# Optimization experiments

Measured on AMD Instinct MI355X. Metric: run time of the kernel, lower is better.

Reference implementation:

```python
import jax, jax.numpy as jnp
import numpy as np

N, E, B, IN, DIM, H = 20000, 320000, 128, 25, 64, 8

def _lin(key, fin, fout):
    k1, k2 = jax.random.split(key)
    s = 1.0 / np.sqrt(fin)
    return (jax.random.uniform(k1, (fin, fout), jnp.float32, -s, s),
            jax.random.uniform(k2, (fout,), jnp.float32, -s, s))

def setup_inputs() -> dict:
    key = jax.random.key(0)
    ks = jax.random.split(key, 12)
    x = jax.random.normal(ks[0], (N, IN), jnp.float32)
    edge_index = jax.random.randint(ks[1], (2, E), 0, N, jnp.int64)
    batch = jnp.sort(jax.random.randint(ks[2], (N,), 0, B, jnp.int64))
    W0, b0 = _lin(ks[3], IN, DIM)
    Wg, _ = _lin(ks[4], DIM, H * DIM)            # GATConv lin (no bias)
    att_src = jax.random.normal(ks[5], (H, DIM), jnp.float32) * (1.0 / np.sqrt(DIM))
    att_dst = jax.random.normal(ks[6], (H, DIM), jnp.float32) * (1.0 / np.sqrt(DIM))
    bg = jnp.zeros((H * DIM,), jnp.float32)       # GATConv output bias
    Wh, bh = _lin(ks[7], H * DIM, DIM)            # head_nn
    sl = 1.0 / np.sqrt(DIM)
    W_ih = jax.random.uniform(ks[8], (4 * DIM, 2 * DIM), jnp.float32, -sl, sl)
    W_hh = jax.random.uniform(ks[9], (4 * DIM, DIM), jnp.float32, -sl, sl)
    b_ih = jnp.zeros((4 * DIM,), jnp.float32)
    b_hh = jnp.zeros((4 * DIM,), jnp.float32)
    W1, b1 = _lin(ks[10], 2 * DIM, DIM)
    W2, b2 = _lin(ks[11], DIM, 1)
    return dict(x=x, edge_index=edge_index, batch=batch, W0=W0, b0=b0, Wg=Wg,
                att_src=att_src, att_dst=att_dst, bg=bg, Wh=Wh, bh=bh,
                W_ih=W_ih, W_hh=W_hh, b_ih=b_ih, b_hh=b_hh, W1=W1, b1=b1, W2=W2, b2=b2)

def _forward(x, edge_index, batch, W0, b0, Wg, att_src, att_dst, bg, Wh, bh,
             W_ih, W_hh, b_ih, b_hh, W1, b1, W2, b2):
    n = x.shape[0]
    h0 = jax.nn.relu(x @ W0 + b0)                         # [N, DIM]
    xh = (h0 @ Wg).reshape(n, H, DIM)                     # [N, H, C]
    # add self-loops (PyG GATConv default)
    loop = jnp.arange(n, dtype=edge_index.dtype)
    src = jnp.concatenate([edge_index[0], loop])
    dst = jnp.concatenate([edge_index[1], loop])
    a_s = jnp.einsum('nhc,hc->nh', xh, att_src)           # [N, H]
    a_d = jnp.einsum('nhc,hc->nh', xh, att_dst)
    e = jax.nn.leaky_relu(a_s[src] + a_d[dst], 0.2)       # [Etot, H]
    m = jax.ops.segment_max(e, dst, num_segments=n)
    w = jnp.exp(e - m[dst])
    s = jax.ops.segment_sum(w, dst, num_segments=n)
    alpha = w / s[dst]                                    # segment softmax over dst
    agg = jax.ops.segment_sum(alpha[:, :, None] * xh[src], dst, num_segments=n)
    out = jax.nn.relu(agg.reshape(n, H * DIM) + bg)
    out = jax.nn.relu(out @ Wh + bh)                      # [N, DIM]
    # Set2Set, 3 processing steps
    q_star = jnp.zeros((B, 2 * DIM), out.dtype)
    h = jnp.zeros((B, DIM), out.dtype)
    c = jnp.zeros((B, DIM), out.dtype)
    for _ in range(3):
        g = q_star @ W_ih.T + b_ih + h @ W_hh.T + b_hh
        i_g, f_g, g_g, o_g = jnp.split(g, 4, axis=-1)
        c = jax.nn.sigmoid(f_g) * c + jax.nn.sigmoid(i_g) * jnp.tanh(g_g)
        h = jax.nn.sigmoid(o_g) * jnp.tanh(c)
        q = h                                             # [B, DIM]
        e2 = jnp.sum(out * q[batch], axis=-1)             # [N]
        m2 = jax.ops.segment_max(e2, batch, num_segments=B)
        w2 = jnp.exp(e2 - m2[batch])
        s2 = jax.ops.segment_sum(w2, batch, num_segments=B)
        a2 = w2 / s2[batch]
        r = jax.ops.segment_sum(a2[:, None] * out, batch, num_segments=B)
        q_star = jnp.concatenate([q, r], axis=-1)
    y = jax.nn.relu(q_star @ W1 + b1)
    y = y @ W2 + b2
    return y.reshape(-1)

def reference(x, edge_index, batch, W0, b0, Wg, att_src, att_dst, bg, Wh, bh,
              W_ih, W_hh, b_ih, b_hh, W1, b1, W2, b2):
    return _forward(x, edge_index, batch, W0, b0, Wg, att_src, att_dst, bg, Wh, bh,
                    W_ih, W_hh, b_ih, b_hh, W1, b1, W2, b2)
```

## Files before the change

### kernel.cpp

```cpp
#include <hip/hip_runtime.h>

#define N_NODES 20000
#define N_EDGES 320000
#define NBATCH  128

typedef __attribute__((ext_vector_type(8))) short s8v;
typedef __attribute__((ext_vector_type(4))) float f32x4;
typedef __attribute__((ext_vector_type(4))) int i32x4;

__device__ __forceinline__ float lrelu(float v) { return v > 0.f ? v : 0.2f * v; }
__device__ __forceinline__ float rdlane(float v, int l) {
    return __int_as_float(__builtin_amdgcn_readlane(__float_as_int(v), l));
}
__device__ __forceinline__ unsigned short bf16_rne(float f) {
    unsigned u = __float_as_uint(f);
    unsigned r = u + 0x7FFF + ((u >> 16) & 1);
    return (unsigned short)(r >> 16);
}

__global__ void k_small(const float* __restrict__ Wg, const float* __restrict__ Wh,
                        const float* __restrict__ att_s, const float* __restrict__ att_d,
                        float* __restrict__ vsd,
                        const int* __restrict__ batch, int* __restrict__ segst,
                        int* __restrict__ deg,
                        unsigned short* __restrict__ wgt_hi, unsigned short* __restrict__ wgt_lo,
                        unsigned short* __restrict__ wht_hi, unsigned short* __restrict__ wht_lo,
                        int n, int b) {
    int tid = threadIdx.x;
    int gid = blockIdx.x * 256 + tid;
    if (gid < n) deg[gid] = 0;
    if (blockIdx.x < 2) {
        int t = blockIdx.x * 256 + tid;
        int k = t >> 3, h = t & 7;
        const float* wrow = Wg + (size_t)k * 512 + h * 64;
        float s1 = 0.f, s2 = 0.f;
        #pragma unroll 8
        for (int c = 0; c < 64; c++) {
            float w = wrow[c];
            s1 += w * att_s[h * 64 + c];
            s2 += w * att_d[h * 64 + c];
        }
        vsd[k * 16 + h] = s1;
        vsd[k * 16 + 8 + h] = s2;
    } else if (blockIdx.x == 2) {
        if (tid > b) return;
        int lo = 0, hi = n;
        while (lo < hi) { int mid = (lo + hi) >> 1; if (batch[mid] < tid) lo = mid + 1; else hi = mid; }
        segst[tid] = lo;
    } else {
        int wi = (blockIdx.x - 3) * 256 + tid;
        int sel = wi >> 15;
        int r = wi & 32767;
        int h = r >> 12, nn = (r >> 6) & 63, k = r & 63;
        float val = (sel == 0) ? Wg[(size_t)k * 512 + h * 64 + nn]
                               : Wh[(size_t)(h * 64 + k) * 64 + nn];
        unsigned short hi = bf16_rne(val);
        float hf = __uint_as_float((unsigned)hi << 16);
        unsigned short lo = bf16_rne(val - hf);
        int o = h * 4096 + nn * 64 + k;
        if (sel == 0) { wgt_hi[o] = hi; wgt_lo[o] = lo; }
        else          { wht_hi[o] = hi; wht_lo[o] = lo; }
    }
}

__global__ void k_h0c(const float* __restrict__ x, const float* __restrict__ W0,
                      const float* __restrict__ b0, float* __restrict__ h0,
                      const int* __restrict__ edst, int* __restrict__ deg, int n) {
    __shared__ float ws[25 * 64];
    __shared__ float bs[64];
    __shared__ float xs[100];
    int t = threadIdx.x;
    if (t < 64) {
        int e = blockIdx.x * 64 + t;
        atomicAdd(&deg[edst[e]], 1);
    }
    for (int i = t; i < 25 * 64; i += 256) ws[i] = W0[i];
    if (t < 64) bs[t] = b0[t];
    int nb = blockIdx.x * 4;
    if (t < 100 && nb * 25 + t < n * 25) xs[t] = x[(size_t)nb * 25 + t];
    __syncthreads();
    int node = nb + (t >> 6);
    int c = t & 63;
    if (node >= n) return;
    float s = bs[c];
    const float* xr = xs + (t >> 6) * 25;
    #pragma unroll
    for (int k = 0; k < 25; k++) s += xr[k] * ws[k * 64 + c];
    h0[(size_t)node * 64 + c] = fmaxf(s, 0.f);
}

__global__ __launch_bounds__(256) void k_asd_scan(const float* __restrict__ h0,
                                                  const float* __restrict__ vsd,
                                                  float* __restrict__ a_s, float* __restrict__ a_d,
                                                  const int* __restrict__ deg,
                                                  int* __restrict__ tmp, int* __restrict__ bsum,
                                                  int nasd, int n) {
    __shared__ float hs[16][65];
    __shared__ float vl[64 * 16];
    __shared__ int wsum[4];
    int tid = threadIdx.x;
    if (blockIdx.x >= nasd) {
        int s = blockIdx.x - nasd;
        int i = s * 256 + tid;
        int lane = tid & 63, w = tid >> 6;
        int v = (i < n) ? deg[i] + 1 : 0;
        int x = v;
        #pragma unroll
        for (int off = 1; off < 64; off <<= 1) {
            int t2 = __shfl_up(x, off);
            if (lane >= off) x += t2;
        }
        if (lane == 63) wsum[w] = x;
        __syncthreads();
        int pre = 0;
        #pragma unroll
        for (int j = 0; j < 4; j++) if (j < w) pre += wsum[j];
        if (i < n) tmp[i] = pre + x - v;
        if (tid == 255) bsum[s] = pre + x;
        return;
    }
    int rbase = blockIdx.x * 16;
    {
        int row = tid / 16, c4 = (tid % 16) * 4;
        float4 hv = *(const float4*)(h0 + (size_t)(rbase + row) * 64 + c4);
        hs[row][c4] = hv.x; hs[row][c4 + 1] = hv.y; hs[row][c4 + 2] = hv.z; hs[row][c4 + 3] = hv.w;
    }
    #pragma unroll
    for (int j = 0; j < 4; j++) vl[tid + j * 256] = vsd[tid + j * 256];
    __syncthreads();
    int nl = tid / 16, o = tid % 16;
    float acc = 0.f;
    #pragma unroll 16
    for (int k = 0; k < 64; k++) acc += hs[nl][k] * vl[k * 16 + o];
    int node = rbase + nl;
    if (o < 8) a_s[node * 8 + o] = acc;
    else       a_d[node * 8 + (o - 8)] = acc;
}

__global__ void k_scan2(const int* __restrict__ tmp, const int* __restrict__ bsum,
                        int* __restrict__ offs, int* __restrict__ adj,
                        int* __restrict__ cursor, int n, int nblk) {
    int i = blockIdx.x * 256 + threadIdx.x;
    if (i > n) return;
    int b = i >> 8;
    int pre = 0;
    for (int j = 0; j < b; j++) pre += bsum[j];
    if (i == n) {
        int tot = pre;
        for (int j = b; j < nblk; j++) tot += bsum[j];
        offs[n] = tot;
        return;
    }
    int o = pre + tmp[i];
    offs[i] = o;
    adj[o] = i;
    cursor[i] = o + 1;
}

__global__ void k_fill_edge(const int* __restrict__ src, const int* __restrict__ dst,
                            int* __restrict__ cursor, int* __restrict__ adj, int e) {
    int i = blockIdx.x * 256 + threadIdx.x;
    if (i >= e) return;
    int p = atomicAdd(&cursor[dst[i]], 1);
    adj[p] = src[i];
}

__global__ __launch_bounds__(256) void k_gat6(const int* __restrict__ offs, const int* __restrict__ adj,
                                              const float* __restrict__ a_s, const float* __restrict__ a_d,
                                              const float* __restrict__ h0,
                                              float* __restrict__ agg_pre, int n) {
    int lane = threadIdx.x & 63;
    int node = blockIdx.x * 4 + (threadIdx.x >> 6);
    if (node >= n) return;
    int beg = offs[node], end = offs[node + 1];
    int g = lane >> 3, h = lane & 7;
    float ad = a_d[node * 8 + h];

    float m = -1e30f, s = 0.f;
    for (int i = beg + g; i < end; i += 8) {
        int src = adj[i];
        float e = lrelu(a_s[src * 8 + h] + ad);
        if (e > m) { s = s * __expf(m - e) + 1.f; m = e; }
        else       { s += __expf(e - m); }
    }
    #pragma unroll
    for (int off = 8; off < 64; off <<= 1) {
        float mo = __shfl_xor(m, off), so = __shfl_xor(s, off);
        float mn = fmaxf(m, mo);
        s = s * __expf(m - mn) + so * __expf(mo - mn);
        m = mn;
    }
    float rcp = 1.f / s;

    float acc[8] = {0.f, 0.f, 0.f, 0.f, 0.f, 0.f, 0.f, 0.f};
    for (int sbase = beg; sbase < end; sbase += 64) {
        int scnt = end - sbase; if (scnt > 64) scnt = 64;
        int srcv = 0;
        if (lane < scnt) srcv = adj[sbase + lane];
        float al[8];
        #pragma unroll
        for (int j = 0; j < 8; j++) {
            int q = j * 8 + g;
            float alv = 0.f;
            if (q < scnt) {
                int sq = __shfl(srcv, q);
                float e = lrelu(a_s[sq * 8 + h] + ad);
                alv = __expf(e - m) * rcp;
            }
            al[j] = alv;
        }
        #pragma unroll
        for (int j = 0; j < 8; j += 2) {
            int qb0 = j * 8, qb1 = (j + 1) * 8;
            if (qb0 >= scnt) break;
            bool has1 = qb1 < scnt;
            int sg0[8], sg1[8];
            float xv0[8], xv1[8];
            #pragma unroll
            for (int g2 = 0; g2 < 8; g2++) sg0[g2] = __builtin_amdgcn_readlane(srcv, qb0 + g2);
            #pragma unroll
            for (int g2 = 0; g2 < 8; g2++) sg1[g2] = __builtin_amdgcn_readlane(srcv, qb1 + g2);
            #pragma unroll
            for (int g2 = 0; g2 < 8; g2++) xv0[g2] = h0[(size_t)sg0[g2] * 64 + lane];
            if (has1) {
                #pragma unroll
                for (int g2 = 0; g2 < 8; g2++) xv1[g2] = h0[(size_t)sg1[g2] * 64 + lane];
            }
            #pragma unroll
            for (int g2 = 0; g2 < 8; g2++) {
                #pragma unroll
                for (int h2 = 0; h2 < 8; h2++)
                    acc[h2] += rdlane(al[j], g2 * 8 + h2) * xv0[g2];
            }
            if (has1) {
                #pragma unroll
                for (int g2 = 0; g2 < 8; g2++) {
                    #pragma unroll
                    for (int h2 = 0; h2 < 8; h2++)
                        acc[h2] += rdlane(al[j + 1], g2 * 8 + h2) * xv1[g2];
                }
            }
        }
    }
    #pragma unroll
    for (int h2 = 0; h2 < 8; h2++)
        agg_pre[(size_t)node * 512 + h2 * 64 + lane] = acc[h2];
}

__global__ __launch_bounds__(64) void k_fmma(const float* __restrict__ agg_pre,
                                             const unsigned short* __restrict__ wgt_hi,
                                             const unsigned short* __restrict__ wgt_lo,
                                             const unsigned short* __restrict__ wht_hi,
                                             const unsigned short* __restrict__ wht_lo,
                                             const float* __restrict__ bg,
                                             float* __restrict__ part, int M) {
    __shared__ unsigned C1[16 * 68];
    int lane = threadIdx.x;
    int m = lane & 15, quad = lane >> 4;
    int r0 = blockIdx.x * 16;
    int pair = blockIdx.y;
    f32x4 accO[4];
    #pragma unroll
    for (int i = 0; i < 4; i++) accO[i] = (f32x4){0.f, 0.f, 0.f, 0.f};

    #pragma unroll
    for (int hh = 0; hh < 2; hh++) {
        int h = pair * 2 + hh;
        s8v ahi[2], alo[2];
        #pragma unroll
        for (int ks = 0; ks < 2; ks++) {
            const float* ap = agg_pre + (size_t)(r0 + m) * 512 + h * 64 + ks * 32 + quad * 8;
            float av[8];
            *(float4*)&av[0] = *(const float4*)ap;
            *(float4*)&av[4] = *(const float4*)(ap + 4);
            #pragma unroll
            for (int j = 0; j < 8; j++) {
                unsigned short hi = bf16_rne(av[j]);
                float hf = __uint_as_float((unsigned)hi << 16);
                unsigned short lo = bf16_rne(av[j] - hf);
                ahi[ks][j] = (short)hi;
                alo[ks][j] = (short)lo;
            }
        }
        #pragma unroll
        for (int tn = 0; tn < 4; tn++) {
            f32x4 acc = (f32x4){0.f, 0.f, 0.f, 0.f};
            #pragma unroll
            for (int ks = 0; ks < 2; ks++) {
                const unsigned short* bp = wgt_hi + h * 4096 + (tn * 16 + m) * 64 + ks * 32 + quad * 8;
                const unsigned short* bl = wgt_lo + h * 4096 + (tn * 16 + m) * 64 + ks * 32 + quad * 8;
                s8v bhf = *(const s8v*)bp;
                s8v blf = *(const s8v*)bl;
                acc = __builtin_amdgcn_mfma_f32_16x16x32_bf16(alo[ks], bhf, acc, 0, 0, 0);
                acc = __builtin_amdgcn_mfma_f32_16x16x32_bf16(ahi[ks], blf, acc, 0, 0, 0);
                acc = __builtin_amdgcn_mfma_f32_16x16x32_bf16(ahi[ks], bhf, acc, 0, 0, 0);
            }
            float bgv = bg[h * 64 + tn * 16 + m];
            #pragma unroll
            for (int r = 0; r < 4; r++) {
                float v = fmaxf(acc[r] + bgv, 0.f);
                unsigned short hi = bf16_rne(v);
                float hf = __uint_as_float((unsigned)hi << 16);
                unsigned short lo = bf16_rne(v - hf);
                C1[(quad * 4 + r) * 68 + tn * 16 + m] = (unsigned)hi | ((unsigned)lo << 16);
            }
        }
        __syncthreads();
        s8v a2h[2], a2l[2];
        #pragma unroll
        for (int ks = 0; ks < 2; ks++) {
            const unsigned* cp = &C1[m * 68 + ks * 32 + quad * 8];
            unsigned uu[8];
            *(i32x4*)&uu[0] = *(const i32x4*)cp;
            *(i32x4*)&uu[4] = *(const i32x4*)(cp + 4);
            #pragma unroll
            for (int j = 0; j < 8; j++) {
                a2h[ks][j] = (short)(uu[j] & 0xFFFFu);
                a2l[ks][j] = (short)(uu[j] >> 16);
            }
        }
        #pragma unroll
        for (int tn = 0; tn < 4; tn++) {
            #pragma unroll
            for (int ks = 0; ks < 2; ks++) {
                const unsigned short* bp = wht_hi + h * 4096 + (tn * 16 + m) * 64 + ks * 32 + quad * 8;
                const unsigned short* bl = wht_lo + h * 4096 + (tn * 16 + m) * 64 + ks * 32 + quad * 8;
                s8v bhf = *(const s8v*)bp;
                s8v blf = *(const s8v*)bl;
                accO[tn] = __builtin_amdgcn_mfma_f32_16x16x32_bf16(a2l[ks], bhf, accO[tn], 0, 0, 0);
                accO[tn] = __builtin_amdgcn_mfma_f32_16x16x32_bf16(a2h[ks], blf, accO[tn], 0, 0, 0);
                accO[tn] = __builtin_amdgcn_mfma_f32_16x16x32_bf16(a2h[ks], bhf, accO[tn], 0, 0, 0);
            }
        }
        __syncthreads();
    }
    float* Cb = part + (size_t)pair * M * 64;
    #pragma unroll
    for (int tn = 0; tn < 4; tn++) {
        #pragma unroll
        for (int r = 0; r < 4; r++) {
            int row = r0 + quad * 4 + r;
            Cb[(size_t)row * 64 + tn * 16 + m] = accO[tn][r];
        }
    }
}

#define SROWS 208
__global__ __launch_bounds__(256) void k_s2s(const float* __restrict__ part,
                                             const float* __restrict__ bh,
                                             const int* __restrict__ segst,
                                             const float* __restrict__ W_ih, const float* __restrict__ W_hh,
                                             const float* __restrict__ b_ih, const float* __restrict__ b_hh,
                                             const float* __restrict__ W1, const float* __restrict__ b1,
                                             const float* __restrict__ W2, const float* __restrict__ b2,
                                             float* __restrict__ out, int M) {
    int b = blockIdx.x, tid = threadIdx.x, lane = tid & 63, w = tid >> 6;
    __shared__ float sc[SROWS * 65];
    __shared__ float wlds[1024];
    __shared__ float hl[64], cl[64], rl_[64];
    __shared__ float red[4];
    __shared__ float gsh[256];
    int beg = segst[b], end = segst[b + 1];
    int nrows = end - beg;
    int ncache = nrows < SROWS ? nrows : SROWS;
    const size_t PS = (size_t)M * 64;
    for (int idx = tid; idx < ncache * 16; idx += 256) {
        int r = idx >> 4, q = idx & 15;
        const float* pb = part + (size_t)(beg + r) * 64 + q * 4;
        float4 v0 = *(const float4*)pb;
        float4 v1 = *(const float4*)(pb + PS);
        float4 v2 = *(const float4*)(pb + 2 * PS);
        float4 v3 = *(const float4*)(pb + 3 * PS);
        float4 bv = *(const float4*)(bh + q * 4);
        float* p = &sc[r * 65 + q * 4];
        p[0] = fmaxf(v0.x + v1.x + v2.x + v3.x + bv.x, 0.f);
        p[1] = fmaxf(v0.y + v1.y + v2.y + v3.y + bv.y, 0.f);
        p[2] = fmaxf(v0.z + v1.z + v2.z + v3.z + bv.z, 0.f);
        p[3] = fmaxf(v0.w + v1.w + v2.w + v3.w + bv.w, 0.f);
    }
    if (tid < 64) { hl[tid] = 0.f; cl[tid] = 0.f; rl_[tid] = 0.f; }
    __syncthreads();

    for (int it = 0; it < 3; it++) {
        {
            float acc = b_ih[tid] + b_hh[tid];
            const float* wi = W_ih + (size_t)tid * 128;
            const float* wh = W_hh + (size_t)tid * 64;
            #pragma unroll 8
            for (int k = 0; k < 64; k++) acc += hl[k] * (wi[k] + wh[k]) + rl_[k] * wi[64 + k];
            gsh[tid] = acc;
        }
        __syncthreads();
        if (tid < 64) {
            float ig = gsh[tid], fg = gsh[64 + tid], gg = gsh[128 + tid], og = gsh[192 + tid];
            float cc = cl[tid];
            float si = 1.f / (1.f + __expf(-ig));
            float sf = 1.f / (1.f + __expf(-fg));
            float so = 1.f / (1.f + __expf(-og));
            float cn = sf * cc + si * tanhf(gg);
            cl[tid] = cn;
            hl[tid] = so * tanhf(cn);
        }
        __syncthreads();
        float ev[4];
        int nr = 0;
        float mloc = -1e30f;
        for (int i = tid; i < nrows; i += 256) {
            float d = 0.f;
            if (i < SROWS) {
                const float* rp = &sc[i * 65];
                #pragma unroll 16
                for (int j = 0; j < 64; j++) d += rp[j] * hl[j];
            } else {
                const float* pb = part + (size_t)(beg + i) * 64;
                for (int j = 0; j < 64; j++) {
                    float v = pb[j] + pb[PS + j] + pb[2 * PS + j] + pb[3 * PS + j] + bh[j];
                    d += fmaxf(v, 0.f) * hl[j];
                }
            }
            ev[nr++] = d;
            mloc = fmaxf(mloc, d);
        }
        #pragma unroll
        for (int off = 1; off < 64; off <<= 1) mloc = fmaxf(mloc, __shfl_xor(mloc, off));
        if (lane == 0) red[w] = mloc;
        __syncthreads();
        float m = fmaxf(fmaxf(red[0], red[1]), fmaxf(red[2], red[3]));
        __syncthreads();
        float sloc = 0.f;
        nr = 0;
        for (int i = tid; i < nrows; i += 256) {
            float wv = __expf(ev[nr++] - m);
            if (i < 1024) wlds[i] = wv;
            sloc += wv;
        }
        #pragma unroll
        for (int off = 1; off < 64; off <<= 1) sloc += __shfl_xor(sloc, off);
        if (lane == 0) red[w] = sloc;
        __syncthreads();
        float sv = red[0] + red[1] + red[2] + red[3];
        float inv = sv > 0.f ? 1.f / sv : 0.f;
        float acc = 0.f;
        for (int i = w; i < nrows; i += 4) {
            float v;
            if (i < SROWS) v = sc[i * 65 + lane];
            else {
                const float* pb = part + (size_t)(beg + i) * 64 + lane;
                v = fmaxf(pb[0] + pb[PS] + pb[2 * PS] + pb[3 * PS] + bh[lane], 0.f);
            }
            acc += wlds[i] * v;
        }
        gsh[w * 64 + lane] = acc;
        __syncthreads();
        if (tid < 64)
            rl_[tid] = (gsh[tid] + gsh[64 + tid] + gsh[128 + tid] + gsh[192 + tid]) * inv;
        __syncthreads();
    }
    if (tid < 64) {
        float t = b1[tid];
        #pragma unroll 8
        for (int k = 0; k < 64; k++)
            t += hl[k] * W1[(size_t)k * 64 + tid] + rl_[k] * W1[(size_t)(64 + k) * 64 + tid];
        t = fmaxf(t, 0.f) * W2[tid];
        #pragma unroll
        for (int off = 32; off > 0; off >>= 1) t += __shfl_xor(t, off);
        if (tid == 0) out[b] = t + b2[0];
    }
}

extern "C" void kernel_launch(void* const* d_in, const int* in_sizes, int n_in,
                              void* d_out, int out_size, void* d_ws, size_t ws_size,
                              hipStream_t stream) {
    const float* x     = (const float*)d_in[0];
    const int*   ei    = (const int*)d_in[1];
    const int*   batch = (const int*)d_in[2];
    const float* W0    = (const float*)d_in[3];
    const float* b0    = (const float*)d_in[4];
    const float* Wg    = (const float*)d_in[5];
    const float* att_s = (const float*)d_in[6];
    const float* att_d = (const float*)d_in[7];
    const float* bg    = (const float*)d_in[8];
    const float* Wh    = (const float*)d_in[9];
    const float* bh    = (const float*)d_in[10];
    const float* W_ih  = (const float*)d_in[11];
    const float* W_hh  = (const float*)d_in[12];
    const float* b_ih  = (const float*)d_in[13];
    const float* b_hh  = (const float*)d_in[14];
    const float* W1    = (const float*)d_in[15];
    const float* b1    = (const float*)d_in[16];
    const float* W2    = (const float*)d_in[17];
    const float* b2    = (const float*)d_in[18];
    float* out = (float*)d_out;

    const int* esrc = ei;
    const int* edst = ei + N_EDGES;

    char* wsb = (char*)d_ws;
    size_t off = 0;
    auto alloc = [&](size_t bytes) {
        void* p = wsb + off;
        off = (off + bytes + 255) & ~(size_t)255;
        return p;
    };
    float* h0      = (float*)alloc((size_t)N_NODES * 64 * 4);
    float* agg_pre = (float*)alloc((size_t)N_NODES * 512 * 4);
    float* part    = (float*)alloc((size_t)4 * N_NODES * 64 * 4);
    float* a_s     = (float*)alloc((size_t)N_NODES * 8 * 4);
    float* a_d     = (float*)alloc((size_t)N_NODES * 8 * 4);
    float* vsd     = (float*)alloc(64 * 16 * 4);
    unsigned short* wgt_hi = (unsigned short*)alloc(32768 * 2);
    unsigned short* wgt_lo = (unsigned short*)alloc(32768 * 2);
    unsigned short* wht_hi = (unsigned short*)alloc(32768 * 2);
    unsigned short* wht_lo = (unsigned short*)alloc(32768 * 2);
    int*   deg     = (int*)alloc((size_t)N_NODES * 4);
    int*   tmp     = (int*)alloc((size_t)N_NODES * 4);
    int*   bsum    = (int*)alloc(128 * 4);
    int*   offs    = (int*)alloc((size_t)(N_NODES + 1) * 4);
    int*   cursor  = (int*)alloc((size_t)N_NODES * 4);
    int*   adj     = (int*)alloc((size_t)(N_EDGES + N_NODES) * 4);
    int*   segst   = (int*)alloc((size_t)(NBATCH + 1) * 4);

    const int nscan = (N_NODES + 255) / 256;
    const int nasd  = N_NODES / 16;

    k_small<<<259, 256, 0, stream>>>(Wg, Wh, att_s, att_d, vsd, batch, segst, deg,
                                     wgt_hi, wgt_lo, wht_hi, wht_lo, N_NODES, NBATCH);
    k_h0c<<<N_NODES / 4, 256, 0, stream>>>(x, W0, b0, h0, edst, deg, N_NODES);
    k_asd_scan<<<nasd + nscan, 256, 0, stream>>>(h0, vsd, a_s, a_d, deg, tmp, bsum, nasd, N_NODES);

    k_scan2<<<(N_NODES + 256) / 256, 256, 0, stream>>>(tmp, bsum, offs, adj, cursor, N_NODES, nscan);
    k_fill_edge<<<(N_EDGES + 255) / 256, 256, 0, stream>>>(esrc, edst, cursor, adj, N_EDGES);

    k_gat6<<<(N_NODES + 3) / 4, 256, 0, stream>>>(offs, adj, a_s, a_d, h0, agg_pre, N_NODES);
    k_fmma<<<dim3(N_NODES / 16, 4), 64, 0, stream>>>(agg_pre, wgt_hi, wgt_lo, wht_hi, wht_lo,
                                                     bg, part, N_NODES);

    k_s2s<<<NBATCH, 256, 0, stream>>>(part, bh, segst, W_ih, W_hh, b_ih, b_hh, W1, b1, W2, b2, out, N_NODES);
}
```

Before: 267.0 us.

## Fuse GAT aggregation with per-head MFMA projection and head reduction via LDS

Merges the edge-aggregation kernel and the two-stage MFMA projection into one 1024-thread block that handles 16 nodes. Each wave aggregates one node into shared memory, then 8 waves each run one head's matmuls, and the per-head partial outputs are summed in LDS with bias and ReLU applied. This removes the 40MB agg_pre round trip and the 4-way partial buffer, and simplifies s2s to read a single finished activation. The cost is a large LDS footprint (about 68KB) and 1024-thread blocks, which limit occupancy and make aggregation waves idle at barriers when node degrees differ.

After: 263.4 us. Within noise of the previous version (-1.3%).

```diff
diff --git a/kernel.cpp b/kernel.cpp
--- a/kernel.cpp
+++ b/kernel.cpp
@@ -165,111 +165,108 @@
     adj[p] = src[i];
 }
 
-__global__ __launch_bounds__(256) void k_gat6(const int* __restrict__ offs, const int* __restrict__ adj,
-                                              const float* __restrict__ a_s, const float* __restrict__ a_d,
-                                              const float* __restrict__ h0,
-                                              float* __restrict__ agg_pre, int n) {
-    int lane = threadIdx.x & 63;
-    int node = blockIdx.x * 4 + (threadIdx.x >> 6);
-    if (node >= n) return;
-    int beg = offs[node], end = offs[node + 1];
-    int g = lane >> 3, h = lane & 7;
-    float ad = a_d[node * 8 + h];
-
-    float m = -1e30f, s = 0.f;
-    for (int i = beg + g; i < end; i += 8) {
-        int src = adj[i];
-        float e = lrelu(a_s[src * 8 + h] + ad);
-        if (e > m) { s = s * __expf(m - e) + 1.f; m = e; }
-        else       { s += __expf(e - m); }
-    }
-    #pragma unroll
-    for (int off = 8; off < 64; off <<= 1) {
-        float mo = __shfl_xor(m, off), so = __shfl_xor(s, off);
-        float mn = fmaxf(m, mo);
-        s = s * __expf(m - mn) + so * __expf(mo - mn);
-        m = mn;
-    }
-    float rcp = 1.f / s;
-
-    float acc[8] = {0.f, 0.f, 0.f, 0.f, 0.f, 0.f, 0.f, 0.f};
-    for (int sbase = beg; sbase < end; sbase += 64) {
-        int scnt = end - sbase; if (scnt > 64) scnt = 64;
-        int srcv = 0;
-        if (lane < scnt) srcv = adj[sbase + lane];
-        float al[8];
-        #pragma unroll
-        for (int j = 0; j < 8; j++) {
-            int q = j * 8 + g;
-            float alv = 0.f;
-            if (q < scnt) {
-                int sq = __shfl(srcv, q);
-                float e = lrelu(a_s[sq * 8 + h] + ad);
-                alv = __expf(e - m) * rcp;
-            }
-            al[j] = alv;
-        }
-        #pragma unroll
-        for (int j = 0; j < 8; j += 2) {
-            int qb0 = j * 8, qb1 = (j + 1) * 8;
-            if (qb0 >= scnt) break;
-            bool has1 = qb1 < scnt;
-            int sg0[8], sg1[8];
-            float xv0[8], xv1[8];
-            #pragma unroll
-            for (int g2 = 0; g2 < 8; g2++) sg0[g2] = __builtin_amdgcn_readlane(srcv, qb0 + g2);
-            #pragma unroll
-            for (int g2 = 0; g2 < 8; g2++) sg1[g2] = __builtin_amdgcn_readlane(srcv, qb1 + g2);
-            #pragma unroll
-            for (int g2 = 0; g2 < 8; g2++) xv0[g2] = h0[(size_t)sg0[g2] * 64 + lane];
-            if (has1) {
+#define ASTR 520
+__global__ __launch_bounds__(1024) void k_gatf(const int* __restrict__ offs, const int* __restrict__ adj,
+                                               const float* __restrict__ a_s, const float* __restrict__ a_d,
+                                               const float* __restrict__ h0,
+                                               const unsigned short* __restrict__ wgt_hi,
+                                               const unsigned short* __restrict__ wgt_lo,
+                                               const unsigned short* __restrict__ wht_hi,
+                                               const unsigned short* __restrict__ wht_lo,
+                                               const float* __restrict__ bg, const float* __restrict__ bh,
+                                               float* __restrict__ out2, int n) {
+    __shared__ float stg[16 * ASTR];
+    __shared__ unsigned C1[8][16 * 68];
+    int tid = threadIdx.x;
+    int lane = tid & 63, wv = tid >> 6;
+    int node = blockIdx.x * 16 + wv;
+
+    {
+        int beg = offs[node], end = offs[node + 1];
+        int g = lane >> 3, h = lane & 7;
+        float ad = a_d[node * 8 + h];
+        float m = -1e30f, s = 0.f;
+        for (int i = beg + g; i < end; i += 8) {
+            int src = adj[i];
+            float e = lrelu(a_s[src * 8 + h] + ad);
+            if (e > m) { s = s * __expf(m - e) + 1.f; m = e; }
+            else       { s += __expf(e - m); }
+        }
+        #pragma unroll
+        for (int off = 8; off < 64; off <<= 1) {
+            float mo = __shfl_xor(m, off), so = __shfl_xor(s, off);
+            float mn = fmaxf(m, mo);
+            s = s * __expf(m - mn) + so * __expf(mo - mn);
+            m = mn;
+        }
+        float rcp = 1.f / s;
+
+        float acc[8] = {0.f, 0.f, 0.f, 0.f, 0.f, 0.f, 0.f, 0.f};
+        for (int sbase = beg; sbase < end; sbase += 64) {
+            int scnt = end - sbase; if (scnt > 64) scnt = 64;
+            int srcv = 0;
+            if (lane < scnt) srcv = adj[sbase + lane];
+            float al[8];
+            #pragma unroll
+            for (int j = 0; j < 8; j++) {
+                int q = j * 8 + g;
+                float alv = 0.f;
+                if (q < scnt) {
+                    int sq = __shfl(srcv, q);
+                    float e = lrelu(a_s[sq * 8 + h] + ad);
+                    alv = __expf(e - m) * rcp;
+                }
+                al[j] = alv;
+            }
+            #pragma unroll
+            for (int j = 0; j < 8; j += 2) {
+                int qb0 = j * 8, qb1 = (j + 1) * 8;
+                if (qb0 >= scnt) break;
+                bool has1 = qb1 < scnt;
+                int sg0[8], sg1[8];
+                float xv0[8], xv1[8];
                 #pragma unroll
-                for (int g2 = 0; g2 < 8; g2++) xv1[g2] = h0[(size_t)sg1[g2] * 64 + lane];
-            }
-            #pragma unroll
-            for (int g2 = 0; g2 < 8; g2++) {
+                for (int g2 = 0; g2 < 8; g2++) sg0[g2] = __builtin_amdgcn_readlane(srcv, qb0 + g2);
                 #pragma unroll
-                for (int h2 = 0; h2 < 8; h2++)
-                    acc[h2] += rdlane(al[j], g2 * 8 + h2) * xv0[g2];
-            }
-            if (has1) {
+                for (int g2 = 0; g2 < 8; g2++) sg1[g2] = __builtin_amdgcn_readlane(srcv, qb1 + g2);
+                #pragma unroll
+                for (int g2 = 0; g2 < 8; g2++) xv0[g2] = h0[(size_t)sg0[g2] * 64 + lane];
+                if (has1) {
+                    #pragma unroll
+                    for (int g2 = 0; g2 < 8; g2++) xv1[g2] = h0[(size_t)sg1[g2] * 64 + lane];
+                }
                 #pragma unroll
                 for (int g2 = 0; g2 < 8; g2++) {
                     #pragma unroll
                     for (int h2 = 0; h2 < 8; h2++)
-                        acc[h2] += rdlane(al[j + 1], g2 * 8 + h2) * xv1[g2];
+                        acc[h2] += rdlane(al[j], g2 * 8 + h2) * xv0[g2];
                 }
-            }
-        }
-    }
-    #pragma unroll
-    for (int h2 = 0; h2 < 8; h2++)
-        agg_pre[(size_t)node * 512 + h2 * 64 + lane] = acc[h2];
-}
-
-__global__ __launch_bounds__(64) void k_fmma(const float* __restrict__ agg_pre,
-                                             const unsigned short* __restrict__ wgt_hi,
-                                             const unsigned short* __restrict__ wgt_lo,
-                                             const unsigned short* __restrict__ wht_hi,
-                                             const unsigned short* __restrict__ wht_lo,
-                                             const float* __restrict__ bg,
-                                             float* __restrict__ part, int M) {
-    __shared__ unsigned C1[16 * 68];
-    int lane = threadIdx.x;
-    int m = lane & 15, quad = lane >> 4;
-    int r0 = blockIdx.x * 16;
-    int pair = blockIdx.y;
+                if (has1) {
+                    #pragma unroll
+                    for (int g2 = 0; g2 < 8; g2++) {
+                        #pragma unroll
+                        for (int h2 = 0; h2 < 8; h2++)
+                            acc[h2] += rdlane(al[j + 1], g2 * 8 + h2) * xv1[g2];
+                    }
+                }
+            }
+        }
+        #pragma unroll
+        for (int h2 = 0; h2 < 8; h2++)
+            stg[wv * ASTR + h2 * 64 + lane] = acc[h2];
+    }
+    __syncthreads();
+
+    int m16 = lane & 15, quad = lane >> 4;
     f32x4 accO[4];
     #pragma unroll
     for (int i = 0; i < 4; i++) accO[i] = (f32x4){0.f, 0.f, 0.f, 0.f};
-
-    #pragma unroll
-    for (int hh = 0; hh < 2; hh++) {
-        int h = pair * 2 + hh;
+    if (wv < 8) {
+        int h = wv;
         s8v ahi[2], alo[2];
         #pragma unroll
         for (int ks = 0; ks < 2; ks++) {
-            const float* ap = agg_pre + (size_t)(r0 + m) * 512 + h * 64 + ks * 32 + quad * 8;
+            const float* ap = &stg[m16 * ASTR + h * 64 + ks * 32 + quad * 8];
             float av[8];
             *(float4*)&av[0] = *(const float4*)ap;
             *(float4*)&av[4] = *(const float4*)(ap + 4);
@@ -282,34 +279,34 @@
                 alo[ks][j] = (short)lo;
             }
         }
+        unsigned* C1w = C1[h];
         #pragma unroll
         for (int tn = 0; tn < 4; tn++) {
             f32x4 acc = (f32x4){0.f, 0.f, 0.f, 0.f};
             #pragma unroll
             for (int ks = 0; ks < 2; ks++) {
-                const unsigned short* bp = wgt_hi + h * 4096 + (tn * 16 + m) * 64 + ks * 32 + quad * 8;
-                const unsigned short* bl = wgt_lo + h * 4096 + (tn * 16 + m) * 64 + ks * 32 + quad * 8;
+                const unsigned short* bp = wgt_hi + h * 4096 + (tn * 16 + m16) * 64 + ks * 32 + quad * 8;
+                const unsigned short* bl = wgt_lo + h * 4096 + (tn * 16 + m16) * 64 + ks * 32 + quad * 8;
                 s8v bhf = *(const s8v*)bp;
                 s8v blf = *(const s8v*)bl;
                 acc = __builtin_amdgcn_mfma_f32_16x16x32_bf16(alo[ks], bhf, acc, 0, 0, 0);
                 acc = __builtin_amdgcn_mfma_f32_16x16x32_bf16(ahi[ks], blf, acc, 0, 0, 0);
                 acc = __builtin_amdgcn_mfma_f32_16x16x32_bf16(ahi[ks], bhf, acc, 0, 0, 0);
             }
-            float bgv = bg[h * 64 + tn * 16 + m];
+            float bgv = bg[h * 64 + tn * 16 + m16];
             #pragma unroll
             for (int r = 0; r < 4; r++) {
                 float v = fmaxf(acc[r] + bgv, 0.f);
                 unsigned short hi = bf16_rne(v);
                 float hf = __uint_as_float((unsigned)hi << 16);
                 unsigned short lo = bf16_rne(v - hf);
-                C1[(quad * 4 + r) * 68 + tn * 16 + m] = (unsigned)hi | ((unsigned)lo << 16);
-            }
-        }
-        __syncthreads();
+                C1w[(quad * 4 + r) * 68 + tn * 16 + m16] = (unsigned)hi | ((unsigned)lo << 16);
+            }
+        }
         s8v a2h[2], a2l[2];
         #pragma unroll
         for (int ks = 0; ks < 2; ks++) {
-            const unsigned* cp = &C1[m * 68 + ks * 32 + quad * 8];
+            const unsigned* cp = &C1w[m16 * 68 + ks * 32 + quad * 8];
             unsigned uu[8];
             *(i32x4*)&uu[0] = *(const i32x4*)cp;
             *(i32x4*)&uu[4] = *(const i32x4*)(cp + 4);
@@ -323,8 +320,8 @@
         for (int tn = 0; tn < 4; tn++) {
             #pragma unroll
             for (int ks = 0; ks < 2; ks++) {
-                const unsigned short* bp = wht_hi + h * 4096 + (tn * 16 + m) * 64 + ks * 32 + quad * 8;
-                const unsigned short* bl = wht_lo + h * 4096 + (tn * 16 + m) * 64 + ks * 32 + quad * 8;
+                const unsigned short* bp = wht_hi + h * 4096 + (tn * 16 + m16) * 64 + ks * 32 + quad * 8;
+                const unsigned short* bl = wht_lo + h * 4096 + (tn * 16 + m16) * 64 + ks * 32 + quad * 8;
                 s8v bhf = *(const s8v*)bp;
                 s8v blf = *(const s8v*)bl;
                 accO[tn] = __builtin_amdgcn_mfma_f32_16x16x32_bf16(a2l[ks], bhf, accO[tn], 0, 0, 0);
@@ -332,28 +329,36 @@
                 accO[tn] = __builtin_amdgcn_mfma_f32_16x16x32_bf16(a2h[ks], bhf, accO[tn], 0, 0, 0);
             }
         }
-        __syncthreads();
-    }
-    float* Cb = part + (size_t)pair * M * 64;
-    #pragma unroll
-    for (int tn = 0; tn < 4; tn++) {
-        #pragma unroll
-        for (int r = 0; r < 4; r++) {
-            int row = r0 + quad * 4 + r;
-            Cb[(size_t)row * 64 + tn * 16 + m] = accO[tn][r];
-        }
+    }
+    __syncthreads();
+    if (wv < 8) {
+        float* Pw = &stg[wv * 1024];
+        #pragma unroll
+        for (int tn = 0; tn < 4; tn++) {
+            #pragma unroll
+            for (int r = 0; r < 4; r++)
+                Pw[(quad * 4 + r) * 64 + tn * 16 + m16] = accO[tn][r];
+        }
+    }
+    __syncthreads();
+
+    {
+        int row = tid >> 6, col = tid & 63;
+        float s = stg[row * 64 + col];
+        #pragma unroll
+        for (int h2 = 1; h2 < 8; h2++) s += stg[h2 * 1024 + row * 64 + col];
+        out2[(size_t)(blockIdx.x * 16 + row) * 64 + col] = fmaxf(s + bh[col], 0.f);
     }
 }
 
 #define SROWS 208
-__global__ __launch_bounds__(256) void k_s2s(const float* __restrict__ part,
-                                             const float* __restrict__ bh,
+__global__ __launch_bounds__(256) void k_s2s(const float* __restrict__ out2,
                                              const int* __restrict__ segst,
                                              const float* __restrict__ W_ih, const float* __restrict__ W_hh,
                                              const float* __restrict__ b_ih, const float* __restrict__ b_hh,
                                              const float* __restrict__ W1, const float* __restrict__ b1,
                                              const float* __restrict__ W2, const float* __restrict__ b2,
-                                             float* __restrict__ out, int M) {
+                                             float* __restrict__ out) {
     int b = blockIdx.x, tid = threadIdx.x, lane = tid & 63, w = tid >> 6;
     __shared__ float sc[SROWS * 65];
     __shared__ float wlds[1024];
@@ -363,20 +368,11 @@
     int beg = segst[b], end = segst[b + 1];
     int nrows = end - beg;
     int ncache = nrows < SROWS ? nrows : SROWS;
-    const size_t PS = (size_t)M * 64;
     for (int idx = tid; idx < ncache * 16; idx += 256) {
         int r = idx >> 4, q = idx & 15;
-        const float* pb = part + (size_t)(beg + r) * 64 + q * 4;
-        float4 v0 = *(const float4*)pb;
-        float4 v1 = *(const float4*)(pb + PS);
-        float4 v2 = *(const float4*)(pb + 2 * PS);
-        float4 v3 = *(const float4*)(pb + 3 * PS);
-        float4 bv = *(const float4*)(bh + q * 4);
+        float4 v = *(const float4*)(out2 + (size_t)(beg + r) * 64 + q * 4);
         float* p = &sc[r * 65 + q * 4];
-        p[0] = fmaxf(v0.x + v1.x + v2.x + v3.x + bv.x, 0.f);
-        p[1] = fmaxf(v0.y + v1.y + v2.y + v3.y + bv.y, 0.f);
-        p[2] = fmaxf(v0.z + v1.z + v2.z + v3.z + bv.z, 0.f);
-        p[3] = fmaxf(v0.w + v1.w + v2.w + v3.w + bv.w, 0.f);
+        p[0] = v.x; p[1] = v.y; p[2] = v.z; p[3] = v.w;
     }
     if (tid < 64) { hl[tid] = 0.f; cl[tid] = 0.f; rl_[tid] = 0.f; }
     __syncthreads();
@@ -412,11 +408,8 @@
                 #pragma unroll 16
                 for (int j = 0; j < 64; j++) d += rp[j] * hl[j];
             } else {
-                const float* pb = part + (size_t)(beg + i) * 64;
-                for (int j = 0; j < 64; j++) {
-                    float v = pb[j] + pb[PS + j] + pb[2 * PS + j] + pb[3 * PS + j] + bh[j];
-                    d += fmaxf(v, 0.f) * hl[j];
-                }
+                const float* rp = out2 + (size_t)(beg + i) * 64;
+                for (int j = 0; j < 64; j++) d += rp[j] * hl[j];
             }
             ev[nr++] = d;
             mloc = fmaxf(mloc, d);
@@ -442,12 +435,7 @@
         float inv = sv > 0.f ? 1.f / sv : 0.f;
         float acc = 0.f;
         for (int i = w; i < nrows; i += 4) {
-            float v;
-            if (i < SROWS) v = sc[i * 65 + lane];
-            else {
-                const float* pb = part + (size_t)(beg + i) * 64 + lane;
-                v = fmaxf(pb[0] + pb[PS] + pb[2 * PS] + pb[3 * PS] + bh[lane], 0.f);
-            }
+            float v = (i < SROWS) ? sc[i * 65 + lane] : out2[(size_t)(beg + i) * 64 + lane];
             acc += wlds[i] * v;
         }
         gsh[w * 64 + lane] = acc;
@@ -503,8 +491,7 @@
         return p;
     };
     float* h0      = (float*)alloc((size_t)N_NODES * 64 * 4);
-    float* agg_pre = (float*)alloc((size_t)N_NODES * 512 * 4);
-    float* part    = (float*)alloc((size_t)4 * N_NODES * 64 * 4);
+    float* out2    = (float*)alloc((size_t)N_NODES * 64 * 4);
     float* a_s     = (float*)alloc((size_t)N_NODES * 8 * 4);
     float* a_d     = (float*)alloc((size_t)N_NODES * 8 * 4);
     float* vsd     = (float*)alloc(64 * 16 * 4);
@@ -531,9 +518,8 @@
     k_scan2<<<(N_NODES + 256) / 256, 256, 0, stream>>>(tmp, bsum, offs, adj, cursor, N_NODES, nscan);
     k_fill_edge<<<(N_EDGES + 255) / 256, 256, 0, stream>>>(esrc, edst, cursor, adj, N_EDGES);
 
-    k_gat6<<<(N_NODES + 3) / 4, 256, 0, stream>>>(offs, adj, a_s, a_d, h0, agg_pre, N_NODES);
-    k_fmma<<<dim3(N_NODES / 16, 4), 64, 0, stream>>>(agg_pre, wgt_hi, wgt_lo, wht_hi, wht_lo,
-                                                     bg, part, N_NODES);
-
-    k_s2s<<<NBATCH, 256, 0, stream>>>(part, bh, segst, W_ih, W_hh, b_ih, b_hh, W1, b1, W2, b2, out, N_NODES);
-}
+    k_gatf<<<N_NODES / 16, 1024, 0, stream>>>(offs, adj, a_s, a_d, h0,
+                                              wgt_hi, wgt_lo, wht_hi, wht_lo, bg, bh, out2, N_NODES);
+
+    k_s2s<<<NBATCH, 256, 0, stream>>>(out2, segst, W_ih, W_hh, b_ih, b_hh, W1, b1, W2, b2, out);
+}
```
